# Kernel optimization log

Hardware: AMD Instinct MI355X
Metric: run time of the kernel (lower is better)

The kernel has to match this reference:

```python
import jax, jax.numpy as jnp
import numpy as np
import math

BS, SL, NE, NH = 4, 2048, 1024, 16
HD = NE // NH  # 64


def setup_inputs() -> dict:
    key = jax.random.key(0)
    ks = jax.random.split(key, 5)
    x = jax.random.normal(ks[0], (BS, SL, NE), dtype=jnp.float32)
    # causal mask: 1 where attending allowed (j <= i), 0 otherwise
    mask = jnp.tril(jnp.ones((SL, SL), dtype=jnp.int32))[None, None, :, :]
    s = 1.0 / math.sqrt(NE)
    Wqkv = jax.random.normal(ks[1], (NE, 3 * NE), dtype=jnp.float32) * s
    bqkv = jax.random.normal(ks[2], (3 * NE,), dtype=jnp.float32) * 0.02
    Wo = jax.random.normal(ks[3], (NE, NE), dtype=jnp.float32) * s
    bo = jax.random.normal(ks[4], (NE,), dtype=jnp.float32) * 0.02
    return {"x": x, "mask": mask, "Wqkv": Wqkv, "bqkv": bqkv, "Wo": Wo, "bo": bo}


def reference(x, mask, Wqkv, bqkv, Wo, bo):
    bs, sl, ne = x.shape
    qkv = x @ Wqkv + bqkv                       # [bs, sl, 3*ne]
    q, k, v = jnp.split(qkv, 3, axis=-1)
    # [bs, sl, ne] -> [bs, nh, sl, hd]
    q = q.reshape(bs, sl, NH, HD).transpose(0, 2, 1, 3)
    k = k.reshape(bs, sl, NH, HD).transpose(0, 2, 1, 3)
    v = v.reshape(bs, sl, NH, HD).transpose(0, 2, 1, 3)
    scale = 1.0 / math.sqrt(HD)
    att = jnp.einsum('bhqd,bhkd->bhqk', q, k) * scale  # [bs, nh, sl, sl]
    att = jnp.where(mask == 0, -jnp.inf, att)
    w = jax.nn.softmax(att, axis=-1)
    y = jnp.einsum('bhqk,bhkd->bhqd', w, v)            # [bs, nh, sl, hd]
    y = y.transpose(0, 2, 1, 3).reshape(bs, sl, ne)
    return y @ Wo + bo
```

## Files before the change

### kernel.cpp

```cpp
#include <hip/hip_runtime.h>

#define BS 4
#define SL 2048
#define NE 1024
#define NH 16
#define HD 64
#define N3 3072

typedef __attribute__((ext_vector_type(8))) __bf16 bf16x8;
typedef __attribute__((ext_vector_type(4))) float f32x4;
typedef __attribute__((ext_vector_type(4))) short s16x4;
typedef unsigned short u16;

__device__ __forceinline__ u16 f2bf(float f) {
  union { float f; unsigned int u; } v; v.f = f;
  unsigned int r = v.u + 0x7FFFu + ((v.u >> 16) & 1u);
  return (u16)(r >> 16);
}
__device__ __forceinline__ int pack_bf2(float a, float b) {
  union { float f; unsigned int u; } x, y; x.f = a; y.f = b;
  return (int)((y.u & 0xFFFF0000u) | (x.u >> 16));
}

__device__ __forceinline__ void gld16(const void* g, void* l) {
#if __has_builtin(__builtin_amdgcn_global_load_lds)
  __builtin_amdgcn_global_load_lds(
      (const __attribute__((address_space(1))) unsigned int*)g,
      (__attribute__((address_space(3))) unsigned int*)l, 16, 0, 0);
#else
  *(int4*)((char*)l + (size_t)(threadIdx.x & 63) * 16) = *(const int4*)g;
#endif
}

__global__ void convert_x(const float* __restrict__ x, u16* __restrict__ xb) {
  int i = (blockIdx.x * 256 + threadIdx.x) * 8;
  float4 f0 = *(const float4*)(x + i);
  float4 f1 = *(const float4*)(x + i + 4);
  union { int4 v; u16 h[8]; } p;
  p.h[0] = f2bf(f0.x); p.h[1] = f2bf(f0.y);
  p.h[2] = f2bf(f0.z); p.h[3] = f2bf(f0.w);
  p.h[4] = f2bf(f1.x); p.h[5] = f2bf(f1.y);
  p.h[6] = f2bf(f1.z); p.h[7] = f2bf(f1.w);
  *(int4*)(xb + i) = p.v;
}

__global__ void transpose_w(const float* __restrict__ W, u16* __restrict__ Wt,
                            int K, int N) {
  __shared__ u16 tile[32][33];
  int bn = blockIdx.x * 32, bk = blockIdx.y * 32;
  int tx = threadIdx.x, ty = threadIdx.y;
  for (int r = 0; r < 32; r += 8)
    tile[ty + r][tx] = f2bf(W[(size_t)(bk + ty + r) * N + bn + tx]);
  __syncthreads();
  for (int r = 0; r < 32; r += 8)
    Wt[(size_t)(bn + ty + r) * K + bk + tx] = tile[tx][ty + r];
}

#define MFMA_G(a, b, c) \
  __builtin_amdgcn_mfma_f32_16x16x32_bf16(a, b, c, 0, 0, 0)

template <int C32>
__global__ __launch_bounds__(256, 2) void gemm2b(
    const u16* __restrict__ A, const u16* __restrict__ Bt,
    const float* __restrict__ bias, void* __restrict__ C, int M, int N, int K,
    int lda) {
  constexpr int BM = 128, BN = 128, BK = 64;
  __shared__ u16 As[2][BM * BK];
  __shared__ u16 Bs[2][BN * BK];

  const int tid = threadIdx.x;
  const int w = tid >> 6, lane = tid & 63;
  const int lq = lane >> 4, lr = lane & 15;
  const int nwx = gridDim.x;
  const int nwg = nwx * gridDim.y;
  const int lin = blockIdx.y * nwx + blockIdx.x;
  const int cpx = nwg >> 3;
  const int swb = (lin & 7) * cpx + (lin >> 3);
  const int m0 = (swb / nwx) * BM, n0 = (swb % nwx) * BN;
  const int wm = (w >> 1) * 64, wn = (w & 1) * 64;

  const int l8 = lane >> 3, lb = lane & 7;
  const int sw8 = (lb ^ l8) * 8;
  const u16* gA = A + (size_t)(m0 + w * 32 + l8) * lda + sw8;
  const u16* gB = Bt + (size_t)(n0 + w * 32 + l8) * K + sw8;

#define STAGE(buf, gpa, gpb)                                  \
  do {                                                        \
    _Pragma("unroll") for (int c = 0; c < 4; c++) {           \
      gld16((gpa) + (size_t)(c * 8) * lda,                    \
            &As[buf][(w * 32 + c * 8) * 64]);                 \
      gld16((gpb) + (size_t)(c * 8) * K,                      \
            &Bs[buf][(w * 32 + c * 8) * 64]);                 \
    }                                                         \
  } while (0)

  const f32x4 fzero = {0.f, 0.f, 0.f, 0.f};
  f32x4 acc[4][4];
#pragma unroll
  for (int i = 0; i < 4; i++)
#pragma unroll
    for (int j = 0; j < 4; j++) acc[i][j] = fzero;

  const int KT = K / BK;
  STAGE(0, gA, gB);
  __syncthreads();
  const u16* gAn = gA + BK;
  const u16* gBn = gB + BK;

  for (int T = 0; T < KT; T++) {
    const int cur = T & 1;
    if (T + 1 < KT) {
      STAGE(cur ^ 1, gAn, gBn);
      gAn += BK;
      gBn += BK;
    }
    __builtin_amdgcn_sched_barrier(0);

    bf16x8 a[4][2], bfr[4][2];
#pragma unroll
    for (int i = 0; i < 4; i++)
#pragma unroll
      for (int ks = 0; ks < 2; ks++) {
        int row = wm + i * 16 + lr;
        a[i][ks] = *(const bf16x8*)
            &As[cur][row * 64 + (((ks * 4 + lq) ^ (lr & 7)) * 8)];
      }
#pragma unroll
    for (int j = 0; j < 4; j++)
#pragma unroll
      for (int ks = 0; ks < 2; ks++) {
        int row = wn + j * 16 + lr;
        bfr[j][ks] = *(const bf16x8*)
            &Bs[cur][row * 64 + (((ks * 4 + lq) ^ (lr & 7)) * 8)];
      }
    __builtin_amdgcn_s_setprio(1);
#pragma unroll
    for (int ks = 0; ks < 2; ks++)
#pragma unroll
      for (int i = 0; i < 4; i++)
#pragma unroll
        for (int j = 0; j < 4; j++)
          acc[i][j] = MFMA_G(a[i][ks], bfr[j][ks], acc[i][j]);
    __builtin_amdgcn_s_setprio(0);
    __syncthreads();
  }
#undef STAGE

#pragma unroll
  for (int j = 0; j < 4; j++) {
    int col = n0 + wn + j * 16 + lr;
    float bv = bias[col];
#pragma unroll
    for (int i = 0; i < 4; i++) {
#pragma unroll
      for (int r = 0; r < 4; r++) {
        int row = m0 + wm + i * 16 + lq * 4 + r;
        float val = acc[i][j][r] + bv;
        if (C32) ((float*)C)[(size_t)row * N + col] = val;
        else     ((u16*)C)[(size_t)row * N + col]   = f2bf(val);
      }
    }
  }
}

#define KSTR 72
#define MFMA16(a, b, c) __builtin_amdgcn_mfma_f32_16x16x32_bf16(a, b, c, 0, 0, 0)
#define MFMA1616(a, b, c) \
  __builtin_amdgcn_mfma_f32_16x16x16bf16_1k(a, b, c, 0, 0, 0)

__device__ __forceinline__ void attn_step(const bf16x8& q0, const bf16x8& q1,
                                          const u16* __restrict__ Kb,
                                          const u16* __restrict__ Vs,
                                          bool diag, int w, int lq, int lr,
                                          f32x4 (&o)[4], float& m_, float& l_) {
  const f32x4 fzero = {0.f, 0.f, 0.f, 0.f};
  const int swz = (lq ^ (lr & 3)) * 8;
  f32x4 s[4];
  __builtin_amdgcn_s_setprio(1);
#pragma unroll
  for (int j = 0; j < 4; j++) {
    int kr = j * 16 + lr;
    bf16x8 kf0 = *(const bf16x8*)&Kb[kr * 32 + swz];
    bf16x8 kf1 = *(const bf16x8*)&Kb[2048 + kr * 32 + swz];
    f32x4 z = MFMA16(kf0, q0, fzero);
    s[j] = MFMA16(kf1, q1, z);
  }
  __builtin_amdgcn_s_setprio(0);
  if (diag) {
    int qloc = w * 16 + lr - 4 * lq;
#pragma unroll
    for (int j = 0; j < 4; j++)
#pragma unroll
      for (int r = 0; r < 4; r++)
        if (16 * j + r > qloc) s[j][r] = -1e30f;
  }
  float mt = s[0][0];
#pragma unroll
  for (int j = 0; j < 4; j++)
#pragma unroll
    for (int r = 0; r < 4; r++) mt = fmaxf(mt, s[j][r]);
  mt = fmaxf(mt, __shfl_xor(mt, 16));
  mt = fmaxf(mt, __shfl_xor(mt, 32));
  float mn = m_;
  if (!__all(mt <= m_ + 64.0f)) {
    mn = fmaxf(m_, mt);
    float alpha = __expf((m_ - mn) * 0.125f);
    m_ = mn;
    l_ *= alpha;
#pragma unroll
    for (int jd = 0; jd < 4; jd++)
#pragma unroll
      for (int r = 0; r < 4; r++) o[jd][r] *= alpha;
  }
  s16x4 pa[4];
  float psum = 0.f;
#pragma unroll
  for (int j = 0; j < 4; j++) {
    float p0 = __expf((s[j][0] - mn) * 0.125f);
    float p1 = __expf((s[j][1] - mn) * 0.125f);
    float p2 = __expf((s[j][2] - mn) * 0.125f);
    float p3 = __expf((s[j][3] - mn) * 0.125f);
    psum += (p0 + p1) + (p2 + p3);
    union { int i[2]; s16x4 v; } pu;
    pu.i[0] = pack_bf2(p0, p1);
    pu.i[1] = pack_bf2(p2, p3);
    pa[j] = pu.v;
  }
  l_ += psum;
  __builtin_amdgcn_s_setprio(1);
#pragma unroll
  for (int jd = 0; jd < 4; jd++) {
    const u16* vrow = &Vs[(jd * 16 + lr) * KSTR + lq * 16];
    union { int4 q; s16x4 h[2]; } va, vb;
    va.q = *(const int4*)vrow;
    vb.q = *(const int4*)(vrow + 8);
    o[jd] = MFMA1616(va.h[0], pa[0], o[jd]);
    o[jd] = MFMA1616(va.h[1], pa[1], o[jd]);
    o[jd] = MFMA1616(vb.h[0], pa[2], o[jd]);
    o[jd] = MFMA1616(vb.h[1], pa[3], o[jd]);
  }
  __builtin_amdgcn_s_setprio(0);
}

__global__ __launch_bounds__(256, 4) void attn_paired(u16* __restrict__ qkv) {
  __shared__ u16 Ks[2][4096];
  __shared__ u16 Vs[64 * KSTR];

  const int tid = threadIdx.x;
  const int w = tid >> 6, lane = tid & 63;
  const int lq = lane >> 4, lr = lane & 15;
  const int bh = blockIdx.x, p = blockIdx.y;
  const int h = bh & (NH - 1), b = bh >> 4;
  const int qt0 = p, qt1 = (SL / 64 - 1) - p;

  u16* base = qkv + (size_t)b * SL * N3;
  const u16* kbase = base + NE + h * HD;

  const int kg_key = lane >> 2;
  const int kg_blk = (lane & 3) ^ (kg_key & 3);
  const int skey = tid & 63, sd0 = (tid >> 6) * 8;
  const int skeyP = ((skey >> 2) & 3) * 16 + (skey >> 4) * 4 + (skey & 3);
  const u16* vrow0 = base + (size_t)skey * N3 + 2 * NE + h * HD + sd0;

#define KPRE(buf, key0)                                                     \
  {                                                                         \
    _Pragma("unroll") for (int t = 0; t < 2; t++) {                         \
      int chunk = w * 2 + t, half = chunk >> 2, kgrp = chunk & 3;           \
      const u16* g = kbase + (size_t)((key0) + kgrp * 16 + kg_key) * N3 +   \
                     half * 32 + kg_blk * 8;                                \
      gld16(g, &Ks[buf][half * 2048 + kgrp * 512]);                         \
    }                                                                       \
  }

  bf16x8 qf[2][2];
#pragma unroll
  for (int half = 0; half < 2; half++) {
    int qt = half ? qt1 : qt0;
    const u16* qrow = base + (size_t)(qt * 64 + w * 16 + lr) * N3 + h * HD;
    qf[half][0] = *(const bf16x8*)(qrow + lq * 8);
    qf[half][1] = *(const bf16x8*)(qrow + 32 + lq * 8);
  }

  const f32x4 fzero = {0.f, 0.f, 0.f, 0.f};
  f32x4 o[2][4];
  float m_[2], l_[2];
#pragma unroll
  for (int half = 0; half < 2; half++) {
    m_[half] = -1e30f;
    l_[half] = 0.f;
#pragma unroll
    for (int jd = 0; jd < 4; jd++) o[half][jd] = fzero;
  }

  KPRE(0, 0);
  int4 v0 = *(const int4*)vrow0;
  int4 v1 = *(const int4*)(vrow0 + 32);

  const int ktend = qt1 + 1;
  for (int kt = 0; kt < ktend; kt++) {
    __syncthreads();
    {
      union { int4 v; u16 u[8]; } t0, t1;
      t0.v = v0; t1.v = v1;
#pragma unroll
      for (int j = 0; j < 8; j++) {
        Vs[(sd0 + j) * KSTR + skeyP] = t0.u[j];
        Vs[(sd0 + 32 + j) * KSTR + skeyP] = t1.u[j];
      }
    }
    __syncthreads();

    if (kt + 1 < ktend) {
      KPRE((kt + 1) & 1, (kt + 1) * 64);
      const u16* nv = vrow0 + (size_t)(kt + 1) * 64 * N3;
      v0 = *(const int4*)nv;
      v1 = *(const int4*)(nv + 32);
    }

    const u16* Kb = &Ks[kt & 1][0];
    attn_step(qf[1][0], qf[1][1], Kb, Vs, kt == qt1, w, lq, lr, o[1], m_[1],
              l_[1]);
    if (kt <= qt0)
      attn_step(qf[0][0], qf[0][1], Kb, Vs, kt == qt0, w, lq, lr, o[0], m_[0],
                l_[0]);
  }

#pragma unroll
  for (int half = 0; half < 2; half++) {
    int qt = half ? qt1 : qt0;
    float lsum = l_[half];
    lsum += __shfl_xor(lsum, 16);
    lsum += __shfl_xor(lsum, 32);
    float inv = 1.0f / lsum;
    u16* yrow = base + (size_t)(qt * 64 + w * 16 + lr) * N3 + h * HD;
#pragma unroll
    for (int jd = 0; jd < 4; jd++) {
      int2 val;
      val.x = (int)(((unsigned)f2bf(o[half][jd][1] * inv) << 16) |
                    f2bf(o[half][jd][0] * inv));
      val.y = (int)(((unsigned)f2bf(o[half][jd][3] * inv) << 16) |
                    f2bf(o[half][jd][2] * inv));
      *(int2*)(yrow + 16 * jd + 4 * lq) = val;
    }
  }
}

extern "C" void kernel_launch(void* const* d_in, const int* in_sizes, int n_in,
                              void* d_out, int out_size, void* d_ws,
                              size_t ws_size, hipStream_t stream) {
  const float* x    = (const float*)d_in[0];
  const float* Wqkv = (const float*)d_in[2];
  const float* bqkv = (const float*)d_in[3];
  const float* Wo   = (const float*)d_in[4];
  const float* bo   = (const float*)d_in[5];

  u16* WqkvT  = (u16*)d_ws;
  u16* WoT    = WqkvT + (size_t)N3 * NE;
  u16* xb     = WoT + (size_t)NE * NE;
  u16* qkvbuf = xb + (size_t)BS * SL * NE;

  convert_x<<<(BS * SL * NE) / (256 * 8), 256, 0, stream>>>(x, xb);
  transpose_w<<<dim3(N3 / 32, NE / 32), dim3(32, 8), 0, stream>>>(Wqkv, WqkvT,
                                                                  NE, N3);
  transpose_w<<<dim3(NE / 32, NE / 32), dim3(32, 8), 0, stream>>>(Wo, WoT, NE,
                                                                  NE);
  gemm2b<0><<<dim3(N3 / 128, (BS * SL) / 128), 256, 0, stream>>>(
      xb, WqkvT, bqkv, qkvbuf, BS * SL, N3, NE, NE);
  attn_paired<<<dim3(BS * NH, SL / 128), 256, 0, stream>>>(qkvbuf);
  gemm2b<1><<<dim3(NE / 128, (BS * SL) / 128), 256, 0, stream>>>(
      qkvbuf, WoT, bo, d_out, BS * SL, NE, NE, N3);
}
```

Baseline: 262.4 us.

## Double-buffer V tile, merge paired q-tile steps, and adjust K swizzle

Double-buffers the V shared-memory tile so the next tile's V write and K prefetch happen before compute, dropping one __syncthreads per iteration. When both query tiles are active, their steps are fused into one routine that reuses the K and V fragment loads and interleaves independent MFMA chains. The K bank swizzle changes to use (row>>1)&3, and the softmax is factored out with a tree max reduction. This costs extra LDS for the second V buffer, which may affect occupancy at 4 blocks per CU, and raises register pressure in the fused path.

```diff
diff --git a/kernel.cpp b/kernel.cpp
--- a/kernel.cpp
+++ b/kernel.cpp
@@ -168,42 +168,20 @@
 #define MFMA1616(a, b, c) \
   __builtin_amdgcn_mfma_f32_16x16x16bf16_1k(a, b, c, 0, 0, 0)
 
-__device__ __forceinline__ void attn_step(const bf16x8& q0, const bf16x8& q1,
-                                          const u16* __restrict__ Kb,
-                                          const u16* __restrict__ Vs,
-                                          bool diag, int w, int lq, int lr,
-                                          f32x4 (&o)[4], float& m_, float& l_) {
-  const f32x4 fzero = {0.f, 0.f, 0.f, 0.f};
-  const int swz = (lq ^ (lr & 3)) * 8;
-  f32x4 s[4];
-  __builtin_amdgcn_s_setprio(1);
-#pragma unroll
-  for (int j = 0; j < 4; j++) {
-    int kr = j * 16 + lr;
-    bf16x8 kf0 = *(const bf16x8*)&Kb[kr * 32 + swz];
-    bf16x8 kf1 = *(const bf16x8*)&Kb[2048 + kr * 32 + swz];
-    f32x4 z = MFMA16(kf0, q0, fzero);
-    s[j] = MFMA16(kf1, q1, z);
-  }
-  __builtin_amdgcn_s_setprio(0);
-  if (diag) {
-    int qloc = w * 16 + lr - 4 * lq;
-#pragma unroll
-    for (int j = 0; j < 4; j++)
-#pragma unroll
-      for (int r = 0; r < 4; r++)
-        if (16 * j + r > qloc) s[j][r] = -1e30f;
-  }
-  float mt = s[0][0];
-#pragma unroll
-  for (int j = 0; j < 4; j++)
-#pragma unroll
-    for (int r = 0; r < 4; r++) mt = fmaxf(mt, s[j][r]);
+__device__ __forceinline__ void softmax_pack(f32x4 (&s)[4], s16x4 (&pa)[4],
+                                             f32x4 (&o)[4], float& m_,
+                                             float& l_) {
+  float a0 = fmaxf(fmaxf(s[0][0], s[0][1]), s[0][2]);
+  float a1 = fmaxf(fmaxf(s[0][3], s[1][0]), s[1][1]);
+  float a2 = fmaxf(fmaxf(s[1][2], s[1][3]), s[2][0]);
+  float a3 = fmaxf(fmaxf(s[2][1], s[2][2]), s[2][3]);
+  float a4 = fmaxf(fmaxf(s[3][0], s[3][1]), s[3][2]);
+  float mt = fmaxf(fmaxf(fmaxf(a0, a1), fmaxf(a2, a3)), fmaxf(a4, s[3][3]));
   mt = fmaxf(mt, __shfl_xor(mt, 16));
   mt = fmaxf(mt, __shfl_xor(mt, 32));
-  float mn = m_;
-  if (!__all(mt <= m_ + 64.0f)) {
-    mn = fmaxf(m_, mt);
+  bool need = !__all(mt <= m_ + 64.0f);
+  float mn = need ? fmaxf(m_, mt) : m_;
+  if (need) {
     float alpha = __expf((m_ - mn) * 0.125f);
     m_ = mn;
     l_ *= alpha;
@@ -212,7 +190,6 @@
 #pragma unroll
       for (int r = 0; r < 4; r++) o[jd][r] *= alpha;
   }
-  s16x4 pa[4];
   float psum = 0.f;
 #pragma unroll
   for (int j = 0; j < 4; j++) {
@@ -227,10 +204,39 @@
     pa[j] = pu.v;
   }
   l_ += psum;
+}
+
+__device__ __forceinline__ void attn_step(const bf16x8& q0, const bf16x8& q1,
+                                          const u16* __restrict__ Kb,
+                                          const u16* __restrict__ Vb,
+                                          bool diag, int qloc, int lq, int lr,
+                                          f32x4 (&o)[4], float& m_, float& l_) {
+  const f32x4 fzero = {0.f, 0.f, 0.f, 0.f};
+  const int swz = (lq ^ ((lr >> 1) & 3)) * 8;
+  f32x4 s[4];
   __builtin_amdgcn_s_setprio(1);
 #pragma unroll
+  for (int j = 0; j < 4; j++) {
+    int kr = j * 16 + lr;
+    bf16x8 kf0 = *(const bf16x8*)&Kb[kr * 32 + swz];
+    bf16x8 kf1 = *(const bf16x8*)&Kb[2048 + kr * 32 + swz];
+    f32x4 z = MFMA16(kf0, q0, fzero);
+    s[j] = MFMA16(kf1, q1, z);
+  }
+  __builtin_amdgcn_s_setprio(0);
+  if (diag) {
+#pragma unroll
+    for (int j = 0; j < 4; j++)
+#pragma unroll
+      for (int r = 0; r < 4; r++)
+        if (16 * j + r > qloc) s[j][r] = -1e30f;
+  }
+  s16x4 pa[4];
+  softmax_pack(s, pa, o, m_, l_);
+  __builtin_amdgcn_s_setprio(1);
+#pragma unroll
   for (int jd = 0; jd < 4; jd++) {
-    const u16* vrow = &Vs[(jd * 16 + lr) * KSTR + lq * 16];
+    const u16* vrow = &Vb[(jd * 16 + lr) * KSTR + lq * 16];
     union { int4 q; s16x4 h[2]; } va, vb;
     va.q = *(const int4*)vrow;
     vb.q = *(const int4*)(vrow + 8);
@@ -242,9 +248,57 @@
   __builtin_amdgcn_s_setprio(0);
 }
 
+__device__ __forceinline__ void attn_step_both(
+    const bf16x8 (&qf)[2][2], const u16* __restrict__ Kb,
+    const u16* __restrict__ Vb, bool diag0, int qloc, int lq, int lr,
+    f32x4 (&o)[2][4], float (&m_)[2], float (&l_)[2]) {
+  const f32x4 fzero = {0.f, 0.f, 0.f, 0.f};
+  const int swz = (lq ^ ((lr >> 1) & 3)) * 8;
+  f32x4 s1[4], s0[4];
+  __builtin_amdgcn_s_setprio(1);
+#pragma unroll
+  for (int j = 0; j < 4; j++) {
+    int kr = j * 16 + lr;
+    bf16x8 kf0 = *(const bf16x8*)&Kb[kr * 32 + swz];
+    bf16x8 kf1 = *(const bf16x8*)&Kb[2048 + kr * 32 + swz];
+    f32x4 z1 = MFMA16(kf0, qf[1][0], fzero);
+    s1[j] = MFMA16(kf1, qf[1][1], z1);
+    f32x4 z0 = MFMA16(kf0, qf[0][0], fzero);
+    s0[j] = MFMA16(kf1, qf[0][1], z0);
+  }
+  __builtin_amdgcn_s_setprio(0);
+  if (diag0) {
+#pragma unroll
+    for (int j = 0; j < 4; j++)
+#pragma unroll
+      for (int r = 0; r < 4; r++)
+        if (16 * j + r > qloc) s0[j][r] = -1e30f;
+  }
+  s16x4 pa1[4], pa0[4];
+  softmax_pack(s1, pa1, o[1], m_[1], l_[1]);
+  softmax_pack(s0, pa0, o[0], m_[0], l_[0]);
+  __builtin_amdgcn_s_setprio(1);
+#pragma unroll
+  for (int jd = 0; jd < 4; jd++) {
+    const u16* vrow = &Vb[(jd * 16 + lr) * KSTR + lq * 16];
+    union { int4 q; s16x4 h[2]; } va, vb;
+    va.q = *(const int4*)vrow;
+    vb.q = *(const int4*)(vrow + 8);
+    o[1][jd] = MFMA1616(va.h[0], pa1[0], o[1][jd]);
+    o[1][jd] = MFMA1616(va.h[1], pa1[1], o[1][jd]);
+    o[1][jd] = MFMA1616(vb.h[0], pa1[2], o[1][jd]);
+    o[1][jd] = MFMA1616(vb.h[1], pa1[3], o[1][jd]);
+    o[0][jd] = MFMA1616(va.h[0], pa0[0], o[0][jd]);
+    o[0][jd] = MFMA1616(va.h[1], pa0[1], o[0][jd]);
+    o[0][jd] = MFMA1616(vb.h[0], pa0[2], o[0][jd]);
+    o[0][jd] = MFMA1616(vb.h[1], pa0[3], o[0][jd]);
+  }
+  __builtin_amdgcn_s_setprio(0);
+}
+
 __global__ __launch_bounds__(256, 4) void attn_paired(u16* __restrict__ qkv) {
   __shared__ u16 Ks[2][4096];
-  __shared__ u16 Vs[64 * KSTR];
+  __shared__ u16 Vs[2][64 * KSTR];
 
   const int tid = threadIdx.x;
   const int w = tid >> 6, lane = tid & 63;
@@ -252,12 +306,13 @@
   const int bh = blockIdx.x, p = blockIdx.y;
   const int h = bh & (NH - 1), b = bh >> 4;
   const int qt0 = p, qt1 = (SL / 64 - 1) - p;
+  const int qloc = w * 16 + lr - 4 * lq;
 
   u16* base = qkv + (size_t)b * SL * N3;
   const u16* kbase = base + NE + h * HD;
 
   const int kg_key = lane >> 2;
-  const int kg_blk = (lane & 3) ^ (kg_key & 3);
+  const int kg_blk = (lane & 3) ^ ((kg_key >> 1) & 3);
   const int skey = tid & 63, sd0 = (tid >> 6) * 8;
   const int skeyP = ((skey >> 2) & 3) * 16 + (skey >> 4) * 4 + (skey & 3);
   const u16* vrow0 = base + (size_t)skey * N3 + 2 * NE + h * HD + sd0;
@@ -271,6 +326,16 @@
       gld16(g, &Ks[buf][half * 2048 + kgrp * 512]);                         \
     }                                                                       \
   }
+#define VWRITE(buf)                                           \
+  {                                                           \
+    union { int4 v; u16 u[8]; } t0, t1;                       \
+    t0.v = v0; t1.v = v1;                                     \
+    u16* Vn = &Vs[buf][0];                                    \
+    _Pragma("unroll") for (int j = 0; j < 8; j++) {           \
+      Vn[(sd0 + j) * KSTR + skeyP] = t0.u[j];                 \
+      Vn[(sd0 + 32 + j) * KSTR + skeyP] = t1.u[j];            \
+    }                                                         \
+  }
 
   bf16x8 qf[2][2];
 #pragma unroll
@@ -295,34 +360,36 @@
   KPRE(0, 0);
   int4 v0 = *(const int4*)vrow0;
   int4 v1 = *(const int4*)(vrow0 + 32);
+  asm volatile("s_waitcnt vmcnt(0)" ::: "memory");
+  VWRITE(0);
+  {
+    const u16* nv = vrow0 + (size_t)64 * N3;
+    v0 = *(const int4*)nv;
+    v1 = *(const int4*)(nv + 32);
+  }
 
   const int ktend = qt1 + 1;
   for (int kt = 0; kt < ktend; kt++) {
     __syncthreads();
-    {
-      union { int4 v; u16 u[8]; } t0, t1;
-      t0.v = v0; t1.v = v1;
-#pragma unroll
-      for (int j = 0; j < 8; j++) {
-        Vs[(sd0 + j) * KSTR + skeyP] = t0.u[j];
-        Vs[(sd0 + 32 + j) * KSTR + skeyP] = t1.u[j];
+    const int nb = (kt + 1) & 1;
+    if (kt + 1 < ktend) {
+      KPRE(nb, (kt + 1) * 64);
+      VWRITE(nb);
+      if (kt + 2 < ktend) {
+        const u16* nv = vrow0 + (size_t)(kt + 2) * 64 * N3;
+        v0 = *(const int4*)nv;
+        v1 = *(const int4*)(nv + 32);
       }
     }
-    __syncthreads();
-
-    if (kt + 1 < ktend) {
-      KPRE((kt + 1) & 1, (kt + 1) * 64);
-      const u16* nv = vrow0 + (size_t)(kt + 1) * 64 * N3;
-      v0 = *(const int4*)nv;
-      v1 = *(const int4*)(nv + 32);
-    }
+    __builtin_amdgcn_sched_barrier(0);
 
     const u16* Kb = &Ks[kt & 1][0];
-    attn_step(qf[1][0], qf[1][1], Kb, Vs, kt == qt1, w, lq, lr, o[1], m_[1],
-              l_[1]);
+    const u16* Vb = &Vs[kt & 1][0];
     if (kt <= qt0)
-      attn_step(qf[0][0], qf[0][1], Kb, Vs, kt == qt0, w, lq, lr, o[0], m_[0],
-                l_[0]);
+      attn_step_both(qf, Kb, Vb, kt == qt0, qloc, lq, lr, o, m_, l_);
+    else
+      attn_step(qf[1][0], qf[1][1], Kb, Vb, kt == qt1, qloc, lq, lr, o[1],
+                m_[1], l_[1]);
   }
 
 #pragma unroll
```

New measurement: 367.7 us. 40.2% more time.
